# Kernel optimization log

Measured on AMD Instinct MI355X. Metric: run time of the kernel, lower is better.

## Reference

```python
import jax, jax.numpy as jnp
import numpy as np

B, L, D, H = 48, 512, 192, 6
DK = D // H
HID = 4 * D
EPS = 1e-5
SCALE = 1.0 / np.float32(np.sqrt(DK))


def _ln(x, g, b):
    mu = x.mean(-1, keepdims=True)
    v = ((x - mu) ** 2).mean(-1, keepdims=True)
    return (x - mu) * jax.lax.rsqrt(v + EPS) * g + b


def _mln(x, m, g, b):
    # masked layernorm: valid rows normalized, invalid rows pass through unchanged
    return jnp.where(m[..., None], _ln(x, g, b), x)


def _mha(q, k, v, mask, wq, bq, wk, bk, wv, bv, wo, bo):
    def proj(x, w, bb):
        return (x @ w + bb).reshape(B, L, H, DK).transpose(0, 2, 1, 3)  # [B,H,L,dk]
    Q, K, V = proj(q, wq, bq), proj(k, wk, bk), proj(v, wv, bv)
    s = jnp.einsum('bhqd,bhkd->bhqk', Q, K) * SCALE
    s = jnp.where(mask[:, None], -1e9, s)  # mask True = invalid pair
    p = jax.nn.softmax(s, axis=-1)
    o = jnp.einsum('bhqk,bhkd->bhqd', p, V).transpose(0, 2, 1, 3).reshape(B, L, D)
    return o @ wo + bo


def _forward(x_a, x_b, valid_a, valid_b,
             ln_a_g, ln_a_b, ln_b_g, ln_b_b, ln_oa_g, ln_oa_b, ln_ob_g, ln_ob_b,
             wq, bq, wk, bk, wv, bv, wo, bo,
             fln_g, fln_b, flno_g, flno_b, w1, b1, w2, b2):
    mB2A = ~(valid_a[:, :, None] & valid_b[:, None, :])  # [B,La,Lb]
    mA2B = ~(valid_b[:, :, None] & valid_a[:, None, :])
    a = _mln(x_a, valid_a, ln_a_g, ln_a_b)
    b = _mln(x_b, valid_b, ln_b_g, ln_b_b)
    oa = _mha(a, b, b, mB2A, wq, bq, wk, bk, wv, bv, wo, bo)
    oa = _mln(oa + x_a, valid_a, ln_oa_g, ln_oa_b)
    ob = _mha(b, a, a, mA2B, wq, bq, wk, bk, wv, bv, wo, bo)
    ob = _mln(ob + x_b, valid_b, ln_ob_g, ln_ob_b)

    def ffn(x, m):
        xn = _mln(x, m, fln_g, fln_b)
        y = jax.nn.gelu(xn @ w1 + b1, approximate=False) @ w2 + b2
        return _mln(x + y, m, flno_g, flno_b)

    return ffn(oa, valid_a), ffn(ob, valid_b)


def setup_inputs() -> dict:
    key = jax.random.key(0)
    ks = jax.random.split(key, 12)
    p = lambda k, s: jax.random.normal(k, s, dtype=jnp.float32) * 0.02
    ones = lambda s: jnp.ones(s, dtype=jnp.float32)
    zeros = lambda s: jnp.zeros(s, dtype=jnp.float32)
    return {
        'x_a': jax.random.normal(ks[0], (B, L, D), dtype=jnp.float32),
        'x_b': jax.random.normal(ks[1], (B, L, D), dtype=jnp.float32),
        'valid_a': jax.random.bernoulli(ks[2], 0.9, (B, L)),
        'valid_b': jax.random.bernoulli(ks[3], 0.9, (B, L)),
        'ln_a_g': ones((D,)), 'ln_a_b': zeros((D,)),
        'ln_b_g': ones((D,)), 'ln_b_b': zeros((D,)),
        'ln_oa_g': ones((D,)), 'ln_oa_b': zeros((D,)),
        'ln_ob_g': ones((D,)), 'ln_ob_b': zeros((D,)),
        'wq': p(ks[4], (D, D)), 'bq': zeros((D,)),
        'wk': p(ks[5], (D, D)), 'bk': zeros((D,)),
        'wv': p(ks[6], (D, D)), 'bv': zeros((D,)),
        'wo': p(ks[7], (D, D)), 'bo': zeros((D,)),
        'fln_g': ones((D,)), 'fln_b': zeros((D,)),
        'flno_g': ones((D,)), 'flno_b': zeros((D,)),
        'w1': p(ks[8], (D, HID)), 'b1': zeros((HID,)),
        'w2': p(ks[9], (HID, D)), 'b2': zeros((D,)),
    }


def reference(x_a, x_b, valid_a, valid_b,
              ln_a_g, ln_a_b, ln_b_g, ln_b_b, ln_oa_g, ln_oa_b, ln_ob_g, ln_ob_b,
              wq, bq, wk, bk, wv, bv, wo, bo,
              fln_g, fln_b, flno_g, flno_b, w1, b1, w2, b2):
    return _forward(x_a, x_b, valid_a, valid_b,
                    ln_a_g, ln_a_b, ln_b_g, ln_b_b, ln_oa_g, ln_oa_b, ln_ob_g, ln_ob_b,
                    wq, bq, wk, bk, wv, bv, wo, bo,
                    fln_g, fln_b, flno_g, flno_b, w1, b1, w2, b2)
```

## Files before the change

### kernel.cpp

```cpp
#include <hip/hip_runtime.h>
#include <math.h>

#define BB 48
#define LL 512
#define DD 192
#define HH 6
#define DKK 32
#define HID 768
#define ROWS (BB * LL)
#define BLD ((size_t)ROWS * DD)
#define SB2 0.25503531f
#define MASKED_X (-36.0f)

typedef unsigned short ushort_t;
typedef unsigned int uint_t;
typedef __bf16 bf16x8 __attribute__((ext_vector_type(8)));
typedef float f32x4 __attribute__((ext_vector_type(4)));

union U4BF8 { uint4 u; bf16x8 b; };
union BFU { __bf16 h; ushort_t u; };

__device__ __forceinline__ ushort_t f2bf(float f) {
  union { float f; uint_t u; } v; v.f = f;
  uint_t r = v.u + 0x7fffu + ((v.u >> 16) & 1u);
  return (ushort_t)(r >> 16);
}
__device__ __forceinline__ ushort_t cvt_bf(float f) {
  BFU c; c.h = (__bf16)f; return c.u;
}

__device__ __forceinline__ int swz_w(int n, int k, int N) {
  return ((k >> 5) * (N >> 4) + (n >> 4)) * 512 +
         ((((k & 31) >> 3) << 4) + (n & 15)) * 8 + (k & 7);
}

__global__ __launch_bounds__(256) void pack_kernel(
    const float* __restrict__ wq, const float* __restrict__ wk,
    const float* __restrict__ wv, const float* __restrict__ wo,
    const float* __restrict__ w1, const float* __restrict__ w2,
    const float* __restrict__ bq, const float* __restrict__ bk,
    const float* __restrict__ bv,
    ushort_t* __restrict__ Wqkv, ushort_t* __restrict__ Wo,
    ushort_t* __restrict__ W1, ushort_t* __restrict__ W2,
    float* __restrict__ bqkv) {
  int i = blockIdx.x * 256 + threadIdx.x;
  if (i < 110592) {
    int n2 = i / 192, k = i - n2 * 192;
    int part = n2 / 192, n = n2 - part * 192;
    const float* src = part == 0 ? wq : (part == 1 ? wk : wv);
    Wqkv[swz_w(n2, k, 576)] = f2bf(src[k * 192 + n]);
  } else if (i < 147456) {
    int j = i - 110592;
    int n = j / 192, k = j - n * 192;
    Wo[swz_w(n, k, 192)] = f2bf(wo[k * 192 + n]);
  } else if (i < 294912) {
    int j = i - 147456;
    int n = j / 192, k = j - n * 192;
    W1[j] = f2bf(w1[k * 768 + n]);
  } else if (i < 442368) {
    int j = i - 294912;
    int n = j / 768, k = j - n * 768;
    W2[j] = f2bf(w2[k * 192 + n]);
  } else if (i < 442944) {
    int j = i - 442368;
    bqkv[j] = j < 192 ? bq[j] : (j < 384 ? bk[j - 192] : bv[j - 384]);
  }
}

__global__ __launch_bounds__(256) void qkv_ln_kernel(
    const float* __restrict__ xa, const float* __restrict__ xb,
    const int* __restrict__ va, const int* __restrict__ vb,
    const float* __restrict__ g_a, const float* __restrict__ b_a,
    const float* __restrict__ g_b, const float* __restrict__ b_b,
    const ushort_t* __restrict__ Wsw, const float* __restrict__ bias,
    ushort_t* __restrict__ QK, ushort_t* __restrict__ Vt) {
  constexpr int N = 576;
  constexpr int CSB = 392;
  __shared__ ushort_t smem[32 * CSB];
  ushort_t* As = smem;

  int tid = threadIdx.x;
  int w = tid >> 6, lane = tid & 63, l15 = lane & 15, kq = lane >> 4;
  int row0 = blockIdx.x * 32;
  int side = row0 >= ROWS;
  int rb = row0 - side * ROWS;
  int batch = rb >> 9;
  int k0 = rb & 511;

  {
    int row = tid >> 3, l8 = tid & 7;
    const float* xr = (side ? xb : xa) + (size_t)(rb + row) * DD + l8 * 24;
    float v[24];
    float s = 0.f;
#pragma unroll
    for (int j = 0; j < 6; ++j) {
      float4 q = *(const float4*)(xr + j * 4);
      v[j*4+0] = q.x; v[j*4+1] = q.y; v[j*4+2] = q.z; v[j*4+3] = q.w;
      s += q.x + q.y + q.z + q.w;
    }
    s += __shfl_xor(s, 1); s += __shfl_xor(s, 2); s += __shfl_xor(s, 4);
    float mu = s * (1.0f / 192.0f);
    float ss = 0.f;
#pragma unroll
    for (int j = 0; j < 24; ++j) { float d = v[j] - mu; ss += d * d; }
    ss += __shfl_xor(ss, 1); ss += __shfl_xor(ss, 2); ss += __shfl_xor(ss, 4);
    float inv = rsqrtf(ss * (1.0f / 192.0f) + 1e-5f);
    int vld = (side ? vb : va)[rb + row];
    const float* g = side ? g_b : g_a;
    const float* be = side ? b_b : b_a;
    ushort_t ob[24];
#pragma unroll
    for (int j = 0; j < 24; ++j) {
      int col = l8 * 24 + j;
      float r = vld ? (v[j] - mu) * inv * g[col] + be[col] : v[j];
      ob[j] = f2bf(r);
    }
#pragma unroll
    for (int j = 0; j < 3; ++j)
      *(uint4*)(&As[row * 200 + l8 * 24 + j * 8]) = *(const uint4*)(&ob[j * 8]);
  }
  __syncthreads();

  f32x4 acc[2][9];
#pragma unroll
  for (int qs = 0; qs < 2; ++qs)
#pragma unroll
    for (int nt = 0; nt < 9; ++nt) acc[qs][nt] = (f32x4){0.f, 0.f, 0.f, 0.f};

#pragma unroll 1
  for (int kk = 0; kk < 6; ++kk) {
    bf16x8 af[2];
#pragma unroll
    for (int qs = 0; qs < 2; ++qs)
      af[qs] = *(const bf16x8*)(&As[(qs * 16 + l15) * 200 + kk * 32 + kq * 8]);
    const ushort_t* wp =
        Wsw + ((size_t)(kk * (N >> 4) + w * 9) << 9) + lane * 8;
#pragma unroll
    for (int nt = 0; nt < 9; ++nt) {
      U4BF8 wf;
      wf.u = *(const uint4*)(wp + (nt << 9));
#pragma unroll
      for (int qs = 0; qs < 2; ++qs)
        acc[qs][nt] = __builtin_amdgcn_mfma_f32_16x16x32_bf16(
            af[qs], wf.b, acc[qs][nt], 0, 0, 0);
    }
  }
  __syncthreads();

  ushort_t* Cs = smem;
#pragma unroll
  for (int nt = 0; nt < 9; ++nt) {
    int t = w * 9 + nt;
    int col = t * 16 + l15;
    float bb = bias[col];
    if (t < 24) {
#pragma unroll
      for (int qs = 0; qs < 2; ++qs)
#pragma unroll
        for (int r = 0; r < 4; ++r)
          Cs[(qs * 16 + kq * 4 + r) * CSB + col] = f2bf(acc[qs][nt][r] + bb);
    } else {
      int vcol = col - 384;
      int h = vcol >> 5, d = vcol & 31;
      size_t vbase = ((size_t)((side * BB + batch) * HH + h) * 32 + d) * 512;
#pragma unroll
      for (int qs = 0; qs < 2; ++qs) {
        ushort_t pk[4];
#pragma unroll
        for (int r = 0; r < 4; ++r) pk[r] = f2bf(acc[qs][nt][r] + bb);
        *(uint2*)(Vt + vbase + k0 + qs * 16 + kq * 4) = *(const uint2*)(&pk[0]);
      }
    }
  }
  __syncthreads();
  constexpr int UPR = 48;
#pragma unroll
  for (int i = 0; i < (32 * UPR) / 256; ++i) {
    int idx = tid + i * 256;
    int r = idx / UPR, u = idx - r * UPR;
    *(uint4*)(QK + (size_t)row0 * 384 + idx * 8) =
        *(const uint4*)(&Cs[r * CSB + u * 8]);
  }
}

__global__ __launch_bounds__(256) void oproj_ln_kernel(
    const ushort_t* __restrict__ A, const ushort_t* __restrict__ Wsw,
    const float* __restrict__ bias,
    const float* __restrict__ xa, const float* __restrict__ xb,
    const int* __restrict__ va, const int* __restrict__ vb,
    const float* __restrict__ g_oa, const float* __restrict__ b_oa,
    const float* __restrict__ g_ob, const float* __restrict__ b_ob,
    const float* __restrict__ g_f, const float* __restrict__ b_f,
    float* __restrict__ outf, ushort_t* __restrict__ outb) {
  __shared__ float smemf[32 * 196];
  ushort_t* As = (ushort_t*)smemf;

  int tid = threadIdx.x;
  int w = tid >> 6, lane = tid & 63, l15 = lane & 15, kq = lane >> 4;
  int row0 = blockIdx.x * 32;
  int side = row0 >= ROWS;
  int rb = row0 - side * ROWS;

  {
    const ushort_t* ap = A + (size_t)row0 * DD;
#pragma unroll
    for (int i = 0; i < 3; ++i) {
      int idx = tid + i * 256;
      int r = idx / 24, c = (idx - r * 24) * 8;
      *(uint4*)(&As[r * 200 + c]) = *(const uint4*)(ap + idx * 8);
    }
  }
  __syncthreads();

  f32x4 acc[2][3];
#pragma unroll
  for (int qs = 0; qs < 2; ++qs)
#pragma unroll
    for (int nt = 0; nt < 3; ++nt) acc[qs][nt] = (f32x4){0.f, 0.f, 0.f, 0.f};

#pragma unroll 1
  for (int kk = 0; kk < 6; ++kk) {
    bf16x8 af[2];
#pragma unroll
    for (int qs = 0; qs < 2; ++qs)
      af[qs] = *(const bf16x8*)(&As[(qs * 16 + l15) * 200 + kk * 32 + kq * 8]);
    const ushort_t* wp =
        Wsw + ((size_t)(kk * (192 >> 4) + w * 3) << 9) + lane * 8;
#pragma unroll
    for (int nt = 0; nt < 3; ++nt) {
      U4BF8 wf;
      wf.u = *(const uint4*)(wp + (nt << 9));
#pragma unroll
      for (int qs = 0; qs < 2; ++qs)
        acc[qs][nt] = __builtin_amdgcn_mfma_f32_16x16x32_bf16(
            af[qs], wf.b, acc[qs][nt], 0, 0, 0);
    }
  }
  __syncthreads();

  float* Cs = smemf;
#pragma unroll
  for (int nt = 0; nt < 3; ++nt) {
    int col = (w * 3 + nt) * 16 + l15;
    float bb = bias[col];
#pragma unroll
    for (int qs = 0; qs < 2; ++qs)
#pragma unroll
      for (int r = 0; r < 4; ++r)
        Cs[(qs * 16 + kq * 4 + r) * 196 + col] = acc[qs][nt][r] + bb;
  }
  __syncthreads();

  int row = tid >> 3, l8 = tid & 7;
  int grow = row0 + row;
  const float* xrow = (side ? xb : xa) + (size_t)(rb + row) * DD;
  const float* crow = &Cs[row * 196];
  float v[24];
  float s = 0.f;
#pragma unroll
  for (int j = 0; j < 6; ++j) {
    int col = j * 32 + l8 * 4;
    float4 q = *(const float4*)(xrow + col);
    v[j*4+0] = crow[col+0] + q.x; v[j*4+1] = crow[col+1] + q.y;
    v[j*4+2] = crow[col+2] + q.z; v[j*4+3] = crow[col+3] + q.w;
    s += v[j*4+0] + v[j*4+1] + v[j*4+2] + v[j*4+3];
  }
  s += __shfl_xor(s, 1); s += __shfl_xor(s, 2); s += __shfl_xor(s, 4);
  float mu = s * (1.0f / 192.0f);
  float ss = 0.f;
#pragma unroll
  for (int j = 0; j < 24; ++j) { float d = v[j] - mu; ss += d * d; }
  ss += __shfl_xor(ss, 1); ss += __shfl_xor(ss, 2); ss += __shfl_xor(ss, 4);
  float inv = rsqrtf(ss * (1.0f / 192.0f) + 1e-5f);
  int vld = (side ? vb : va)[rb + row];
  const float* g1 = side ? g_ob : g_oa;
  const float* b1 = side ? b_ob : b_oa;
  float y[24];
#pragma unroll
  for (int j = 0; j < 6; ++j) {
#pragma unroll
    for (int e = 0; e < 4; ++e) {
      int col = j * 32 + l8 * 4 + e;
      float vv = v[j * 4 + e];
      y[j * 4 + e] = vld ? (vv - mu) * inv * g1[col] + b1[col] : vv;
    }
  }
  float* orow = outf + (size_t)grow * DD;
#pragma unroll
  for (int j = 0; j < 6; ++j) {
    float4 q = {y[j*4+0], y[j*4+1], y[j*4+2], y[j*4+3]};
    *(float4*)(orow + j * 32 + l8 * 4) = q;
  }
  float s2 = 0.f;
#pragma unroll
  for (int j = 0; j < 24; ++j) s2 += y[j];
  s2 += __shfl_xor(s2, 1); s2 += __shfl_xor(s2, 2); s2 += __shfl_xor(s2, 4);
  float mu2 = s2 * (1.0f / 192.0f);
  float ss2 = 0.f;
#pragma unroll
  for (int j = 0; j < 24; ++j) { float e = y[j] - mu2; ss2 += e * e; }
  ss2 += __shfl_xor(ss2, 1); ss2 += __shfl_xor(ss2, 2); ss2 += __shfl_xor(ss2, 4);
  float inv2 = rsqrtf(ss2 * (1.0f / 192.0f) + 1e-5f);
  ushort_t* obrow = outb + (size_t)grow * DD;
#pragma unroll
  for (int j = 0; j < 6; ++j) {
    ushort_t zb[4];
#pragma unroll
    for (int e = 0; e < 4; ++e) {
      int col = j * 32 + l8 * 4 + e;
      float z = vld ? (y[j*4+e] - mu2) * inv2 * g_f[col] + b_f[col] : y[j*4+e];
      zb[e] = f2bf(z);
    }
    *(uint2*)(obrow + j * 32 + l8 * 4) = *(const uint2*)(&zb[0]);
  }
}

__global__ __launch_bounds__(256, 3) void ffn_fused_kernel(
    const ushort_t* __restrict__ A, const ushort_t* __restrict__ W1t,
    const float* __restrict__ bias1, const ushort_t* __restrict__ W2t,
    const float* __restrict__ bias2,
    const int* __restrict__ va, const int* __restrict__ vb,
    const float* __restrict__ g_f, const float* __restrict__ b_f,
    float* __restrict__ outf) {
  __shared__ float smemf[64 * 196];
  ushort_t* As = (ushort_t*)smemf;
  ushort_t* Hs = As + 64 * 200;

  int tid = threadIdx.x;
  int w = tid >> 6;
  int lane = tid & 63;
  int l15 = lane & 15;
  int kq = lane >> 4;
  int row0 = blockIdx.x * 64;
  int side = row0 >= ROWS;
  int rb0 = row0 - side * ROWS;

#pragma unroll
  for (int i = 0; i < 6; ++i) {
    int idx = tid + i * 256;
    int r = idx / 24, c = (idx % 24) * 8;
    *(uint4*)(&As[r * 200 + c]) = *(const uint4*)(A + (size_t)(row0 + r) * DD + c);
  }

  const ushort_t* w1p = W1t + (size_t)(w * 16 + l15) * DD + kq * 8;
  const ushort_t* w2p = W2t + (size_t)(w * 48 + l15) * HID + kq * 8;

  U4BF8 w1f[6], w1n[6], w2f[6];
#pragma unroll
  for (int kk = 0; kk < 6; ++kk)
    w1f[kk].u = *(const uint4*)(w1p + kk * 32);

  f32x4 Cacc[4][3];
#pragma unroll
  for (int qs = 0; qs < 4; ++qs)
#pragma unroll
    for (int nt = 0; nt < 3; ++nt) Cacc[qs][nt] = (f32x4){0.f, 0.f, 0.f, 0.f};

  __syncthreads();

  for (int hc = 0; hc < 12; ++hc) {
#pragma unroll
    for (int kk2 = 0; kk2 < 2; ++kk2)
#pragma unroll
      for (int nt = 0; nt < 3; ++nt)
        w2f[kk2 * 3 + nt].u =
            *(const uint4*)(w2p + (size_t)(nt * 16) * HID + hc * 64 + kk2 * 32);

    f32x4 Hacc[4];
#pragma unroll
    for (int qs = 0; qs < 4; ++qs) Hacc[qs] = (f32x4){0.f, 0.f, 0.f, 0.f};
#pragma unroll
    for (int kk = 0; kk < 6; ++kk) {
#pragma unroll
      for (int qs = 0; qs < 4; ++qs) {
        bf16x8 af = *(const bf16x8*)(&As[(qs * 16 + l15) * 200 + kk * 32 + kq * 8]);
        Hacc[qs] = __builtin_amdgcn_mfma_f32_16x16x32_bf16(
            af, w1f[kk].b, Hacc[qs], 0, 0, 0);
      }
    }

    if (hc < 11) {
#pragma unroll
      for (int kk = 0; kk < 6; ++kk)
        w1n[kk].u = *(const uint4*)(w1p + (size_t)(hc + 1) * 64 * DD + kk * 32);
    }

    {
      float bb = bias1[hc * 64 + w * 16 + l15];
      ushort_t* hb = &Hs[(hc & 1) * 4608];
#pragma unroll
      for (int qs = 0; qs < 4; ++qs)
#pragma unroll
        for (int r = 0; r < 4; ++r) {
          float x = Hacc[qs][r] + bb;
          x = 0.5f * x * (1.0f + erff(x * 0.70710678118654752f));
          hb[(qs * 16 + kq * 4 + r) * 72 + w * 16 + l15] = f2bf(x);
        }
    }
    __syncthreads();

#pragma unroll
    for (int kk2 = 0; kk2 < 2; ++kk2) {
      bf16x8 hf[4];
#pragma unroll
      for (int qs = 0; qs < 4; ++qs)
        hf[qs] = *(const bf16x8*)(&Hs[(hc & 1) * 4608 +
                                      (qs * 16 + l15) * 72 + kk2 * 32 + kq * 8]);
#pragma unroll
      for (int nt = 0; nt < 3; ++nt)
#pragma unroll
        for (int qs = 0; qs < 4; ++qs)
          Cacc[qs][nt] = __builtin_amdgcn_mfma_f32_16x16x32_bf16(
              hf[qs], w2f[kk2 * 3 + nt].b, Cacc[qs][nt], 0, 0, 0);
    }

#pragma unroll
    for (int kk = 0; kk < 6; ++kk) w1f[kk] = w1n[kk];
  }
  __syncthreads();

  float* Cs = smemf;
#pragma unroll
  for (int qs = 0; qs < 4; ++qs)
#pragma unroll
    for (int nt = 0; nt < 3; ++nt) {
      int col = w * 48 + nt * 16 + l15;
      float bb = bias2[col];
#pragma unroll
      for (int r = 0; r < 4; ++r)
        Cs[(qs * 16 + kq * 4 + r) * 196 + col] = Cacc[qs][nt][r] + bb;
    }
  __syncthreads();

  int row = tid >> 2, l4 = tid & 3;
  int grow = row0 + row;
  float* orow = outf + (size_t)grow * DD;
  const float* crow = &Cs[row * 196];
  float v[48];
  float s = 0.f;
#pragma unroll
  for (int j = 0; j < 12; ++j) {
    int col = j * 16 + l4 * 4;
    float4 q = *(const float4*)(orow + col);
    v[j*4+0] = crow[col+0] + q.x; v[j*4+1] = crow[col+1] + q.y;
    v[j*4+2] = crow[col+2] + q.z; v[j*4+3] = crow[col+3] + q.w;
    s += v[j*4+0] + v[j*4+1] + v[j*4+2] + v[j*4+3];
  }
  s += __shfl_xor(s, 1); s += __shfl_xor(s, 2);
  float mu = s * (1.0f / 192.0f);
  float ss = 0.f;
#pragma unroll
  for (int j = 0; j < 48; ++j) { float d = v[j] - mu; ss += d * d; }
  ss += __shfl_xor(ss, 1); ss += __shfl_xor(ss, 2);
  float inv = rsqrtf(ss * (1.0f / 192.0f) + 1e-5f);
  int vld = (side ? vb : va)[rb0 + row];
#pragma unroll
  for (int j = 0; j < 12; ++j) {
    int col = j * 16 + l4 * 4;
    float4 q;
#pragma unroll
    for (int e = 0; e < 4; ++e) {
      float vv = v[j * 4 + e];
      ((float*)&q)[e] = vld ? (vv - mu) * inv * g_f[col + e] + b_f[col + e] : vv;
    }
    *(float4*)(orow + col) = q;
  }
}

__global__ __launch_bounds__(256) void attn_mfma_kernel(
    const ushort_t* __restrict__ QK, const ushort_t* __restrict__ Vt,
    const int* __restrict__ valid_a, const int* __restrict__ valid_b,
    ushort_t* __restrict__ out) {
  int i = blockIdx.x;
  int gid = ((i >> 5) << 3) | (i & 7);
  int qt = (i >> 3) & 3;
  int side = gid >= BB * HH;
  int grem = side ? gid - BB * HH : gid;
  int h = grem % HH;
  int batch = grem / HH;
  int tid = threadIdx.x;
  int w = tid >> 6;
  int lane = tid & 63;
  int l15 = lane & 15;
  int kq = lane >> 4;

  const int* validq = side ? valid_b : valid_a;
  const int* validk = side ? valid_a : valid_b;
  size_t qrow0  = (size_t)side * ROWS + (size_t)batch * LL;
  size_t kvrow0 = (size_t)(1 - side) * ROWS + (size_t)batch * LL;
  const ushort_t* vtp =
      Vt + ((size_t)(((1 - side) * BB + batch) * HH + h) * 32) * 512;

  __shared__ ushort_t Ps[4][32 * 72];

  int qbase = qt * 128 + w * 32;

  U4BF8 qfrag[2];
#pragma unroll
  for (int qs = 0; qs < 2; ++qs)
    qfrag[qs].u = *(const uint4*)(QK + (qrow0 + qbase + qs * 16 + l15) * 384 +
                                  h * DKK + kq * 8);

  float sqf[2][4], mq[2][4];
#pragma unroll
  for (int qs = 0; qs < 2; ++qs)
#pragma unroll
    for (int r = 0; r < 4; ++r) {
      int vq = validq[batch * LL + qbase + qs * 16 + kq * 4 + r];
      sqf[qs][r] = vq ? SB2 : 0.0f;
      mq[qs][r]  = vq ? 0.0f : MASKED_X;
    }

  float lsum[2][4];
  f32x4 Oacc[2][2];
#pragma unroll
  for (int qs = 0; qs < 2; ++qs) {
#pragma unroll
    for (int r = 0; r < 4; ++r) lsum[qs][r] = 0.0f;
#pragma unroll
    for (int ds = 0; ds < 2; ++ds) Oacc[qs][ds] = (f32x4){0.f, 0.f, 0.f, 0.f};
  }

  for (int c = 0; c < LL; c += 64) {
    f32x4 S[2][4];
    float mkb[4];
#pragma unroll
    for (int ks = 0; ks < 4; ++ks) {
      U4BF8 kf;
      kf.u = *(const uint4*)(QK + (kvrow0 + c + ks * 16 + l15) * 384 +
                             192 + h * DKK + kq * 8);
      mkb[ks] = validk[batch * LL + c + ks * 16 + l15] ? 0.0f : MASKED_X;
#pragma unroll
      for (int qs = 0; qs < 2; ++qs) {
        f32x4 z = (f32x4){0.f, 0.f, 0.f, 0.f};
        S[qs][ks] = __builtin_amdgcn_mfma_f32_16x16x32_bf16(
            qfrag[qs].b, kf.b, z, 0, 0, 0);
      }
    }

#pragma unroll
    for (int qs = 0; qs < 2; ++qs)
#pragma unroll
      for (int ks = 0; ks < 4; ++ks)
#pragma unroll
        for (int r = 0; r < 4; ++r) {
          float xs = fmaf(S[qs][ks][r], sqf[qs][r], fminf(mq[qs][r], mkb[ks]));
          float p = __builtin_amdgcn_exp2f(xs);
          lsum[qs][r] += p;
          Ps[w][(qs * 16 + kq * 4 + r) * 72 + ks * 16 + l15] = cvt_bf(p);
        }

#pragma unroll
    for (int kh = 0; kh < 2; ++kh) {
      bf16x8 pf[2], vf[2];
#pragma unroll
      for (int qs = 0; qs < 2; ++qs)
        pf[qs] = *(const bf16x8*)(&Ps[w][(qs * 16 + l15) * 72 + kh * 32 + kq * 8]);
#pragma unroll
      for (int ds = 0; ds < 2; ++ds)
        vf[ds] = *(const bf16x8*)(vtp + (size_t)(ds * 16 + l15) * 512 +
                                  c + kh * 32 + kq * 8);
#pragma unroll
      for (int qs = 0; qs < 2; ++qs)
#pragma unroll
        for (int ds = 0; ds < 2; ++ds)
          Oacc[qs][ds] = __builtin_amdgcn_mfma_f32_16x16x32_bf16(
              pf[qs], vf[ds], Oacc[qs][ds], 0, 0, 0);
    }
  }

#pragma unroll
  for (int qs = 0; qs < 2; ++qs)
#pragma unroll
    for (int r = 0; r < 4; ++r) {
      float sm = lsum[qs][r];
#pragma unroll
      for (int off = 1; off < 16; off <<= 1) sm += __shfl_xor(sm, off);
      lsum[qs][r] = sm;
    }

#pragma unroll
  for (int qs = 0; qs < 2; ++qs)
#pragma unroll
    for (int ds = 0; ds < 2; ++ds)
#pragma unroll
      for (int r = 0; r < 4; ++r) {
        int q = qbase + qs * 16 + kq * 4 + r;
        out[(qrow0 + q) * DD + h * DKK + ds * 16 + l15] =
            f2bf(Oacc[qs][ds][r] / lsum[qs][r]);
      }
}

extern "C" void kernel_launch(void* const* d_in, const int* in_sizes, int n_in,
                              void* d_out, int out_size, void* d_ws, size_t ws_size,
                              hipStream_t stream) {
  const float* x_a = (const float*)d_in[0];
  const float* x_b = (const float*)d_in[1];
  const int* valid_a = (const int*)d_in[2];
  const int* valid_b = (const int*)d_in[3];
  const float* ln_a_g = (const float*)d_in[4];
  const float* ln_a_b = (const float*)d_in[5];
  const float* ln_b_g = (const float*)d_in[6];
  const float* ln_b_b = (const float*)d_in[7];
  const float* ln_oa_g = (const float*)d_in[8];
  const float* ln_oa_b = (const float*)d_in[9];
  const float* ln_ob_g = (const float*)d_in[10];
  const float* ln_ob_b = (const float*)d_in[11];
  const float* wq = (const float*)d_in[12];
  const float* bq = (const float*)d_in[13];
  const float* wk = (const float*)d_in[14];
  const float* bk = (const float*)d_in[15];
  const float* wv = (const float*)d_in[16];
  const float* bv = (const float*)d_in[17];
  const float* wo = (const float*)d_in[18];
  const float* bo = (const float*)d_in[19];
  const float* fln_g = (const float*)d_in[20];
  const float* fln_b = (const float*)d_in[21];
  const float* flno_g = (const float*)d_in[22];
  const float* flno_b = (const float*)d_in[23];
  const float* w1 = (const float*)d_in[24];
  const float* b1 = (const float*)d_in[25];
  const float* w2 = (const float*)d_in[26];
  const float* b2 = (const float*)d_in[27];

  char* wsb = (char*)d_ws;
  ushort_t* Wqkv = (ushort_t*)wsb;
  ushort_t* Wo_t = Wqkv + 110592;
  ushort_t* W1_t = Wo_t + 36864;
  ushort_t* W2_t = W1_t + 147456;
  float*    bqkv = (float*)(W2_t + 147456);
  ushort_t* lnFull = (ushort_t*)(wsb + 887040);
  ushort_t* attO   = lnFull;
  ushort_t* QK = (ushort_t*)(wsb + 19761408);
  ushort_t* Vt = (ushort_t*)(wsb + 57510144);

  float* out_a = (float*)d_out;

  dim3 b256(256);
  dim3 gGemm(2 * ROWS / 32);
  dim3 gAttn(BB * HH * 4 * 2);
  dim3 gFFN(2 * ROWS / 64);

  hipLaunchKernelGGL(pack_kernel, dim3(1731), b256, 0, stream,
                     wq, wk, wv, wo, w1, w2, bq, bk, bv,
                     Wqkv, Wo_t, W1_t, W2_t, bqkv);

  hipLaunchKernelGGL(qkv_ln_kernel, gGemm, b256, 0, stream,
                     x_a, x_b, valid_a, valid_b,
                     ln_a_g, ln_a_b, ln_b_g, ln_b_b,
                     Wqkv, bqkv, QK, Vt);

  hipLaunchKernelGGL(attn_mfma_kernel, gAttn, b256, 0, stream,
                     QK, Vt, valid_a, valid_b, attO);

  hipLaunchKernelGGL(oproj_ln_kernel, gGemm, b256, 0, stream,
                     attO, Wo_t, bo, x_a, x_b, valid_a, valid_b,
                     ln_oa_g, ln_oa_b, ln_ob_g, ln_ob_b, fln_g, fln_b,
                     out_a, lnFull);

  hipLaunchKernelGGL(ffn_fused_kernel, gFFN, b256, 0, stream,
                     lnFull, W1_t, b1, W2_t, b2, valid_a, valid_b,
                     flno_g, flno_b, out_a);
}
```

Baseline: 391.1 us.

## Compute transposed scores and shuffle packed P to registers instead of LDS

The attention kernel now computes S^T (K as the A operand, Q as B), so each lane holds a single query column and the key mask loads as one int4. Probabilities are packed to bf16 pairs with v_cvt_pk_bf16_f32 and rearranged into the PV MFMA operand layout with cross-lane shuffles, which removes the per-wave LDS P buffer. The row-sum reduction shrinks to two xor shuffles. The cost is many ds_bpermute shuffles and selects in place of LDS stores and loads.

```diff
diff --git a/kernel.cpp b/kernel.cpp
--- a/kernel.cpp
+++ b/kernel.cpp
@@ -27,6 +27,11 @@
 }
 __device__ __forceinline__ ushort_t cvt_bf(float f) {
   BFU c; c.h = (__bf16)f; return c.u;
+}
+__device__ __forceinline__ uint_t cvtpk(float lo, float hi) {
+  uint_t d;
+  asm("v_cvt_pk_bf16_f32 %0, %1, %2" : "=v"(d) : "v"(lo), "v"(hi));
+  return d;
 }
 
 __device__ __forceinline__ int swz_w(int n, int k, int N) {
@@ -491,103 +496,106 @@
   const ushort_t* vtp =
       Vt + ((size_t)(((1 - side) * BB + batch) * HH + h) * 32) * 512;
 
-  __shared__ ushort_t Ps[4][32 * 72];
-
   int qbase = qt * 128 + w * 32;
 
   U4BF8 qfrag[2];
 #pragma unroll
-  for (int qs = 0; qs < 2; ++qs)
-    qfrag[qs].u = *(const uint4*)(QK + (qrow0 + qbase + qs * 16 + l15) * 384 +
-                                  h * DKK + kq * 8);
-
-  float sqf[2][4], mq[2][4];
-#pragma unroll
-  for (int qs = 0; qs < 2; ++qs)
-#pragma unroll
-    for (int r = 0; r < 4; ++r) {
-      int vq = validq[batch * LL + qbase + qs * 16 + kq * 4 + r];
-      sqf[qs][r] = vq ? SB2 : 0.0f;
-      mq[qs][r]  = vq ? 0.0f : MASKED_X;
-    }
-
-  float lsum[2][4];
+  for (int g = 0; g < 2; ++g)
+    qfrag[g].u = *(const uint4*)(QK + (qrow0 + qbase + g * 16 + l15) * 384 +
+                                 h * DKK + kq * 8);
+
+  float sqf[2], mq[2];
+#pragma unroll
+  for (int g = 0; g < 2; ++g) {
+    int vq = validq[batch * LL + qbase + g * 16 + l15];
+    sqf[g] = vq ? SB2 : 0.0f;
+    mq[g]  = vq ? 0.0f : MASKED_X;
+  }
+
+  float lsum[2] = {0.f, 0.f};
   f32x4 Oacc[2][2];
 #pragma unroll
-  for (int qs = 0; qs < 2; ++qs) {
-#pragma unroll
-    for (int r = 0; r < 4; ++r) lsum[qs][r] = 0.0f;
-#pragma unroll
-    for (int ds = 0; ds < 2; ++ds) Oacc[qs][ds] = (f32x4){0.f, 0.f, 0.f, 0.f};
-  }
+  for (int g = 0; g < 2; ++g)
+#pragma unroll
+    for (int ds = 0; ds < 2; ++ds) Oacc[g][ds] = (f32x4){0.f, 0.f, 0.f, 0.f};
+
+  int slA = l15 + ((kq & 1) << 5);
+  int slB = slA + 16;
+  int hi = kq >> 1;
 
   for (int c = 0; c < LL; c += 64) {
-    f32x4 S[2][4];
-    float mkb[4];
-#pragma unroll
-    for (int ks = 0; ks < 4; ++ks) {
+    uint_t pk[2][4][2];
+#pragma unroll
+    for (int t = 0; t < 4; ++t) {
       U4BF8 kf;
-      kf.u = *(const uint4*)(QK + (kvrow0 + c + ks * 16 + l15) * 384 +
+      kf.u = *(const uint4*)(QK + (kvrow0 + c + t * 16 + l15) * 384 +
                              192 + h * DKK + kq * 8);
-      mkb[ks] = validk[batch * LL + c + ks * 16 + l15] ? 0.0f : MASKED_X;
-#pragma unroll
-      for (int qs = 0; qs < 2; ++qs) {
-        f32x4 z = (f32x4){0.f, 0.f, 0.f, 0.f};
-        S[qs][ks] = __builtin_amdgcn_mfma_f32_16x16x32_bf16(
-            qfrag[qs].b, kf.b, z, 0, 0, 0);
+      int4 vk = *(const int4*)(validk + batch * LL + c + t * 16 + kq * 4);
+      f32x4 z = (f32x4){0.f, 0.f, 0.f, 0.f};
+      f32x4 S0 = __builtin_amdgcn_mfma_f32_16x16x32_bf16(kf.b, qfrag[0].b, z, 0, 0, 0);
+      f32x4 S1 = __builtin_amdgcn_mfma_f32_16x16x32_bf16(kf.b, qfrag[1].b, z, 0, 0, 0);
+      float mkb[4];
+      mkb[0] = vk.x ? 0.0f : MASKED_X;
+      mkb[1] = vk.y ? 0.0f : MASKED_X;
+      mkb[2] = vk.z ? 0.0f : MASKED_X;
+      mkb[3] = vk.w ? 0.0f : MASKED_X;
+      float p0[4], p1[4];
+#pragma unroll
+      for (int r = 0; r < 4; ++r) {
+        p0[r] = __builtin_amdgcn_exp2f(fmaf(S0[r], sqf[0], fminf(mq[0], mkb[r])));
+        p1[r] = __builtin_amdgcn_exp2f(fmaf(S1[r], sqf[1], fminf(mq[1], mkb[r])));
+        lsum[0] += p0[r];
+        lsum[1] += p1[r];
       }
-    }
-
-#pragma unroll
-    for (int qs = 0; qs < 2; ++qs)
-#pragma unroll
-      for (int ks = 0; ks < 4; ++ks)
-#pragma unroll
-        for (int r = 0; r < 4; ++r) {
-          float xs = fmaf(S[qs][ks][r], sqf[qs][r], fminf(mq[qs][r], mkb[ks]));
-          float p = __builtin_amdgcn_exp2f(xs);
-          lsum[qs][r] += p;
-          Ps[w][(qs * 16 + kq * 4 + r) * 72 + ks * 16 + l15] = cvt_bf(p);
+      pk[0][t][0] = cvtpk(p0[0], p0[1]); pk[0][t][1] = cvtpk(p0[2], p0[3]);
+      pk[1][t][0] = cvtpk(p1[0], p1[1]); pk[1][t][1] = cvtpk(p1[2], p1[3]);
+    }
+
+#pragma unroll
+    for (int cc = 0; cc < 2; ++cc) {
+      U4BF8 pa[2];
+#pragma unroll
+      for (int g = 0; g < 2; ++g) {
+        uint_t d[4];
+#pragma unroll
+        for (int j = 0; j < 4; ++j) {
+          int sl = (j < 2) ? slA : slB;
+          uint_t v0 = (uint_t)__shfl((int)pk[g][2 * cc][j & 1], sl, 64);
+          uint_t v1 = (uint_t)__shfl((int)pk[g][2 * cc + 1][j & 1], sl, 64);
+          d[j] = hi ? v1 : v0;
         }
-
-#pragma unroll
-    for (int kh = 0; kh < 2; ++kh) {
-      bf16x8 pf[2], vf[2];
-#pragma unroll
-      for (int qs = 0; qs < 2; ++qs)
-        pf[qs] = *(const bf16x8*)(&Ps[w][(qs * 16 + l15) * 72 + kh * 32 + kq * 8]);
+        pa[g].u = make_uint4(d[0], d[1], d[2], d[3]);
+      }
+      bf16x8 vf[2];
 #pragma unroll
       for (int ds = 0; ds < 2; ++ds)
         vf[ds] = *(const bf16x8*)(vtp + (size_t)(ds * 16 + l15) * 512 +
-                                  c + kh * 32 + kq * 8);
-#pragma unroll
-      for (int qs = 0; qs < 2; ++qs)
+                                  c + cc * 32 + kq * 8);
+#pragma unroll
+      for (int g = 0; g < 2; ++g)
 #pragma unroll
         for (int ds = 0; ds < 2; ++ds)
-          Oacc[qs][ds] = __builtin_amdgcn_mfma_f32_16x16x32_bf16(
-              pf[qs], vf[ds], Oacc[qs][ds], 0, 0, 0);
-    }
-  }
-
-#pragma unroll
-  for (int qs = 0; qs < 2; ++qs)
-#pragma unroll
-    for (int r = 0; r < 4; ++r) {
-      float sm = lsum[qs][r];
-#pragma unroll
-      for (int off = 1; off < 16; off <<= 1) sm += __shfl_xor(sm, off);
-      lsum[qs][r] = sm;
-    }
-
-#pragma unroll
-  for (int qs = 0; qs < 2; ++qs)
+          Oacc[g][ds] = __builtin_amdgcn_mfma_f32_16x16x32_bf16(
+              pa[g].b, vf[ds], Oacc[g][ds], 0, 0, 0);
+    }
+  }
+
+#pragma unroll
+  for (int g = 0; g < 2; ++g) {
+    lsum[g] += __shfl_xor(lsum[g], 16);
+    lsum[g] += __shfl_xor(lsum[g], 32);
+  }
+
+#pragma unroll
+  for (int g = 0; g < 2; ++g)
 #pragma unroll
     for (int ds = 0; ds < 2; ++ds)
 #pragma unroll
       for (int r = 0; r < 4; ++r) {
-        int q = qbase + qs * 16 + kq * 4 + r;
+        float ls = __shfl(lsum[g], kq * 4 + r, 64);
+        int q = qbase + g * 16 + kq * 4 + r;
         out[(qrow0 + q) * DD + h * DKK + ds * 16 + l15] =
-            f2bf(Oacc[qs][ds][r] / lsum[qs][r]);
+            f2bf(Oacc[g][ds][r] / ls);
       }
 }
 
```

After: 390.6 us. Within noise of the previous version (-0.1%).
